# Performance work log

Measured on AMD Instinct MI355X. Metric: run time of the kernel, lower is better.

Reference implementation:

```python
import jax, jax.numpy as jnp
import numpy as np

TAU = 2.0      # LIF membrane time constant
ALPHA = 4.0    # spikingjelly surrogate.Sigmoid default alpha
EPS = 1e-5     # BatchNorm eps
HEADS = 8

@jax.custom_vjp
def heaviside(x):
    return (x >= 0).astype(x.dtype)

def _hv_fwd(x):
    return (x >= 0).astype(x.dtype), x

def _hv_bwd(x, g):
    s = jax.nn.sigmoid(ALPHA * x)
    return (g * ALPHA * s * (1.0 - s),)

heaviside.defvjp(_hv_fwd, _hv_bwd)

def lif(x, vth=1.0):
    # multi-step LIF, decay_input=True, v_reset=0 (hard reset), detach_reset=True
    def step(v, xt):
        v = v + (xt - v) / TAU
        s = heaviside(v - vth)
        v = v * (1.0 - jax.lax.stop_gradient(s))
        return v, s
    _, spikes = jax.lax.scan(step, jnp.zeros_like(x[0]), x)
    return spikes

def bn(x, gamma, beta, mean, var):
    # x: [T,B,C,N]; eval-mode BatchNorm1d over channel axis 2
    inv = gamma * jax.lax.rsqrt(var + EPS)
    return x * inv[None, None, :, None] + (beta - mean * inv)[None, None, :, None]

def conv1x1(x, w):
    # x: [T,B,C,N], w: [Cout,Cin] (Conv1d kernel_size=1)
    return jnp.einsum('tbcn,dc->tbdn', x, w)

def setup_inputs():
    key = jax.random.key(0)
    ks = jax.random.split(key, 24)
    T, B, C, H, W = 4, 16, 512, 32, 32
    scale = 1.0 / np.sqrt(C)
    d = {}
    d['x'] = jax.random.normal(ks[0], (T, B, C, H, W), jnp.float32)
    def bn_params(i):
        g = 1.0 + 0.1 * jax.random.normal(ks[i], (C,), jnp.float32)
        b = 0.1 * jax.random.normal(ks[i + 1], (C,), jnp.float32)
        m = 0.1 * jax.random.normal(ks[i + 2], (C,), jnp.float32)
        v = jax.random.uniform(ks[i + 3], (C,), jnp.float32, 0.5, 1.5)
        return g, b, m, v
    d['q_w'] = scale * jax.random.normal(ks[1], (C, C), jnp.float32)
    d['q_gamma'], d['q_beta'], d['q_mean'], d['q_var'] = bn_params(2)
    d['k_w'] = scale * jax.random.normal(ks[6], (C, C), jnp.float32)
    d['k_gamma'], d['k_beta'], d['k_mean'], d['k_var'] = bn_params(7)
    d['proj_w'] = scale * jax.random.normal(ks[11], (C, C), jnp.float32)
    d['proj_b'] = 0.01 * jax.random.normal(ks[12], (C,), jnp.float32)
    d['p_gamma'], d['p_beta'], d['p_mean'], d['p_var'] = bn_params(13)
    return d

def reference(x, q_w, q_gamma, q_beta, q_mean, q_var,
              k_w, k_gamma, k_beta, k_mean, k_var,
              proj_w, proj_b, p_gamma, p_beta, p_mean, p_var):
    T, B, C, H, W = x.shape
    N = H * W
    Dh = C // HEADS
    xs = lif(x).reshape(T, B, C, N)                    # shortcut_lif then flatten(3)
    q = lif(bn(conv1x1(xs, q_w), q_gamma, q_beta, q_mean, q_var))
    k = lif(bn(conv1x1(xs, k_w), k_gamma, k_beta, k_mean, k_var))
    qh = q.reshape(T, B, HEADS, Dh, N).sum(axis=3, keepdims=True)  # [T,B,h,1,N]
    attn = lif(qh, vth=0.5)
    kh = k.reshape(T, B, HEADS, Dh, N)
    y = (attn * kh).reshape(T, B, C, N)
    y = bn(conv1x1(y, proj_w) + proj_b[None, None, :, None],
           p_gamma, p_beta, p_mean, p_var)
    return y.reshape(T, B, C, H, W), attn
```

## Files before the change

### kernel.cpp

```cpp
#include <hip/hip_runtime.h>

typedef unsigned char u8;
typedef unsigned short u16;
typedef unsigned int u32;
typedef float f32x4 __attribute__((ext_vector_type(4)));
typedef short s16x8 __attribute__((ext_vector_type(8)));

#define T_ 4
#define B_ 16
#define C_ 512
#define N_ 1024
#define YSZ 33554432

__device__ __forceinline__ u16 f2bf(float f) {
  u32 u = __float_as_uint(f);
  u32 r = u + 0x7FFFu + ((u >> 16) & 1u);
  return (u16)(r >> 16);
}
__device__ __forceinline__ float bf2f(u16 h) { return __uint_as_float(((u32)h) << 16); }

__device__ __forceinline__ void async16(const void* g, void* l) {
  __builtin_amdgcn_global_load_lds((const __attribute__((address_space(1))) void*)g,
                                   (__attribute__((address_space(3))) void*)l, 16, 0, 0);
}

__device__ __forceinline__ s16x8 expand8(u32 m) {
  union { u32 w[4]; s16x8 v; } u;
  u.w[0] = (m & 1u   ? 0x3F80u : 0u) | (m & 2u   ? 0x3F800000u : 0u);
  u.w[1] = (m & 4u   ? 0x3F80u : 0u) | (m & 8u   ? 0x3F800000u : 0u);
  u.w[2] = (m & 16u  ? 0x3F80u : 0u) | (m & 32u  ? 0x3F800000u : 0u);
  u.w[3] = (m & 64u  ? 0x3F80u : 0u) | (m & 128u ? 0x3F800000u : 0u);
  return u.v;
}

__global__ void prep_kernel(const float* __restrict__ qw, const float* __restrict__ kw,
                            const float* __restrict__ pw,
                            const float* __restrict__ qg, const float* __restrict__ qb,
                            const float* __restrict__ qm, const float* __restrict__ qv,
                            const float* __restrict__ kg, const float* __restrict__ kb,
                            const float* __restrict__ km, const float* __restrict__ kv,
                            const float* __restrict__ pg, const float* __restrict__ pbt,
                            const float* __restrict__ pm, const float* __restrict__ pv,
                            u16* __restrict__ whlq, u16* __restrict__ whlk,
                            u16* __restrict__ pwb, float* __restrict__ consts) {
  int blk = blockIdx.x, tid = threadIdx.x;
  if (blk < 512) {
    int d = blk;
    for (int c = tid; c < 512; c += 256) {
      float w = qw[d * 512 + c];
      u16 hi = f2bf(w);
      whlq[d * 1024 + c] = hi;
      whlq[d * 1024 + 512 + c] = f2bf(w - bf2f(hi));
      w = kw[d * 512 + c];
      hi = f2bf(w);
      whlk[d * 1024 + c] = hi;
      whlk[d * 1024 + 512 + c] = f2bf(w - bf2f(hi));
      pwb[d * 512 + c] = f2bf(pw[d * 512 + c]);
    }
  } else {
    for (int c = tid; c < 512; c += 256) {
      float inv = qg[c] / sqrtf(qv[c] + 1e-5f);
      consts[c] = inv; consts[512 + c] = qb[c] - qm[c] * inv;
      inv = kg[c] / sqrtf(kv[c] + 1e-5f);
      consts[1024 + c] = inv; consts[1536 + c] = kb[c] - km[c] * inv;
      inv = pg[c] / sqrtf(pv[c] + 1e-5f);
      consts[2048 + c] = inv; consts[2560 + c] = pbt[c] - pm[c] * inv;
    }
  }
}

__global__ __launch_bounds__(256) void lifx_kernel(const float* __restrict__ x,
                                                   u8* __restrict__ xsb) {
  int b = blockIdx.z;
  int cbase = blockIdx.y * 64, nbase = blockIdx.x * 64;
  int tid = threadIdx.x;
  int c_l = tid >> 6, n_l = tid & 63;
  float v[16];
#pragma unroll
  for (int i = 0; i < 16; ++i) v[i] = 0.f;
  for (int t = 0; t < 4; ++t) {
    const float* xp = x + ((size_t)(t * 16 + b) * 512 + cbase + c_l * 16) * 1024 + nbase + n_l;
    u32 mask = 0;
#pragma unroll
    for (int i = 0; i < 16; ++i) {
      float xv = xp[(size_t)i * 1024];
      float vn = v[i] + 0.5f * (xv - v[i]);
      bool s = vn >= 1.0f;
      mask |= (s ? 1u : 0u) << i;
      v[i] = s ? 0.f : vn;
    }
    *(u16*)&xsb[((size_t)(t * 16 + b) * 1024 + nbase + n_l) * 64 + (cbase >> 3) + c_l * 2] =
        (u16)mask;
  }
}

__global__ __launch_bounds__(256, 4) void gemm_q_kernel(
    const u16* __restrict__ A, const u8* __restrict__ xsb,
    const float* __restrict__ consts, float* __restrict__ dout) {
  const int tid = threadIdx.x;
  const int lane = tid & 63, w = tid >> 6;
  const int quad = lane >> 4, l16 = lane & 15;
  const int b = blockIdx.z;
  const int m_blk = blockIdx.y * 64, n_blk = blockIdx.x * 128;
  const int srow = lane >> 3;
  const int scol = (((lane & 7) ^ srow) & 7) * 8;
  __shared__ __align__(16) u16 smem[2 * 4096];
  u16* Ash = smem;
  u16* Asl = smem + 4096;
  const int rxor = l16 & 7;
  const int row0 = n_blk + w * 32 + l16;
  const int row1 = row0 + 16;
  float v[32];
#pragma unroll
  for (int i = 0; i < 32; ++i) v[i] = 0.f;
  float va[2] = {0.f, 0.f};

  for (int t = 0; t < 4; ++t) {
    f32x4 acc[4][2];
    const f32x4 zero = {0.f, 0.f, 0.f, 0.f};
#pragma unroll
    for (int i = 0; i < 4; ++i)
#pragma unroll
      for (int j = 0; j < 2; ++j) acc[i][j] = zero;
    const u8* bitsT = xsb + (size_t)(t * 16 + b) * (N_ * 64);

    for (int k0 = 0; k0 < 512; k0 += 64) {
#pragma unroll
      for (int i = 0; i < 2; ++i) {
        int r = i * 32 + w * 8 + srow;
        int lo = (i * 32 + w * 8) * 64;
        async16(A + (size_t)(m_blk + r) * 1024 + k0 + scol, &Ash[lo]);
        async16(A + (size_t)(m_blk + r) * 1024 + 512 + k0 + scol, &Asl[lo]);
      }
      uint2 g0 = *(const uint2*)&bitsT[(size_t)row0 * 64 + (k0 >> 3)];
      uint2 g1 = *(const uint2*)&bitsT[(size_t)row1 * 64 + (k0 >> 3)];
      __syncthreads();
#pragma unroll
      for (int kk = 0; kk < 2; ++kk) {
        s16x8 ah[4], al[4], bf[2];
        const int slot = ((kk * 4 + quad) ^ rxor) * 8;
#pragma unroll
        for (int ti = 0; ti < 4; ++ti) {
          ah[ti] = *(const s16x8*)&Ash[(ti * 16 + l16) * 64 + slot];
          al[ti] = *(const s16x8*)&Asl[(ti * 16 + l16) * 64 + slot];
        }
        u32 w0 = kk ? g0.y : g0.x;
        u32 w1 = kk ? g1.y : g1.x;
        bf[0] = expand8((w0 >> (quad * 8)) & 0xFFu);
        bf[1] = expand8((w1 >> (quad * 8)) & 0xFFu);
#pragma unroll
        for (int ti = 0; ti < 4; ++ti)
#pragma unroll
          for (int tj = 0; tj < 2; ++tj) {
            acc[ti][tj] = __builtin_amdgcn_mfma_f32_16x16x32_bf16(ah[ti], bf[tj], acc[ti][tj], 0, 0, 0);
            acc[ti][tj] = __builtin_amdgcn_mfma_f32_16x16x32_bf16(al[ti], bf[tj], acc[ti][tj], 0, 0, 0);
          }
      }
      __syncthreads();
    }

    float qp[2] = {0.f, 0.f};
#pragma unroll
    for (int ti = 0; ti < 4; ++ti) {
#pragma unroll
      for (int r = 0; r < 4; ++r) {
        int row = m_blk + ti * 16 + quad * 4 + r;
        float iv = consts[row], ib = consts[512 + row];
#pragma unroll
        for (int tj = 0; tj < 2; ++tj) {
          float bnv = acc[ti][tj][r] * iv + ib;
          float vv = v[(ti * 2 + tj) * 4 + r];
          float vn = vv + 0.5f * (bnv - vv);
          bool s = vn >= 1.0f;
          v[(ti * 2 + tj) * 4 + r] = s ? 0.f : vn;
          qp[tj] += s ? 1.f : 0.f;
        }
      }
    }
    int h = m_blk >> 6;
#pragma unroll
    for (int tj = 0; tj < 2; ++tj) {
      float q = qp[tj];
      q += __shfl_xor(q, 16, 64);
      q += __shfl_xor(q, 32, 64);
      float vn = va[tj] + 0.5f * (q - va[tj]);
      bool s = vn >= 0.5f;
      va[tj] = s ? 0.f : vn;
      if (quad == 0) {
        int col = n_blk + w * 32 + tj * 16 + l16;
        dout[(size_t)YSZ + ((size_t)(t * 16 + b) * 8 + h) * 1024 + col] = s ? 1.f : 0.f;
      }
    }
  }
}

__global__ __launch_bounds__(256, 4) void gemm_k_kernel(
    const u16* __restrict__ A, const u8* __restrict__ xsb,
    const float* __restrict__ consts, const float* __restrict__ dout,
    u8* __restrict__ y2b) {
  const int tid = threadIdx.x;
  const int lane = tid & 63, w = tid >> 6;
  const int quad = lane >> 4, l16 = lane & 15;
  const int b = blockIdx.z;
  const int m_blk = blockIdx.y * 64, n_blk = blockIdx.x * 128;
  const int srow = lane >> 3;
  const int scol = (((lane & 7) ^ srow) & 7) * 8;
  __shared__ __align__(16) u16 smem[9216];
  u16* Ash = smem;
  u16* Asl = smem + 4096;
  u16* Ys  = smem;
  const int rxor = l16 & 7;
  const int row0 = n_blk + w * 32 + l16;
  const int row1 = row0 + 16;
  float v[32];
#pragma unroll
  for (int i = 0; i < 32; ++i) v[i] = 0.f;

  for (int t = 0; t < 4; ++t) {
    f32x4 acc[4][2];
    const f32x4 zero = {0.f, 0.f, 0.f, 0.f};
#pragma unroll
    for (int i = 0; i < 4; ++i)
#pragma unroll
      for (int j = 0; j < 2; ++j) acc[i][j] = zero;
    const u8* bitsT = xsb + (size_t)(t * 16 + b) * (N_ * 64);

    for (int k0 = 0; k0 < 512; k0 += 64) {
#pragma unroll
      for (int i = 0; i < 2; ++i) {
        int r = i * 32 + w * 8 + srow;
        int lo = (i * 32 + w * 8) * 64;
        async16(A + (size_t)(m_blk + r) * 1024 + k0 + scol, &Ash[lo]);
        async16(A + (size_t)(m_blk + r) * 1024 + 512 + k0 + scol, &Asl[lo]);
      }
      uint2 g0 = *(const uint2*)&bitsT[(size_t)row0 * 64 + (k0 >> 3)];
      uint2 g1 = *(const uint2*)&bitsT[(size_t)row1 * 64 + (k0 >> 3)];
      __syncthreads();
#pragma unroll
      for (int kk = 0; kk < 2; ++kk) {
        s16x8 ah[4], al[4], bf[2];
        const int slot = ((kk * 4 + quad) ^ rxor) * 8;
#pragma unroll
        for (int ti = 0; ti < 4; ++ti) {
          ah[ti] = *(const s16x8*)&Ash[(ti * 16 + l16) * 64 + slot];
          al[ti] = *(const s16x8*)&Asl[(ti * 16 + l16) * 64 + slot];
        }
        u32 w0 = kk ? g0.y : g0.x;
        u32 w1 = kk ? g1.y : g1.x;
        bf[0] = expand8((w0 >> (quad * 8)) & 0xFFu);
        bf[1] = expand8((w1 >> (quad * 8)) & 0xFFu);
#pragma unroll
        for (int ti = 0; ti < 4; ++ti)
#pragma unroll
          for (int tj = 0; tj < 2; ++tj) {
            acc[ti][tj] = __builtin_amdgcn_mfma_f32_16x16x32_bf16(ah[ti], bf[tj], acc[ti][tj], 0, 0, 0);
            acc[ti][tj] = __builtin_amdgcn_mfma_f32_16x16x32_bf16(al[ti], bf[tj], acc[ti][tj], 0, 0, 0);
          }
      }
      __syncthreads();
    }

    int h = m_blk >> 6;
    float at[2];
#pragma unroll
    for (int tj = 0; tj < 2; ++tj) {
      int col = n_blk + w * 32 + tj * 16 + l16;
      at[tj] = dout[(size_t)YSZ + ((size_t)(t * 16 + b) * 8 + h) * 1024 + col];
    }

#pragma unroll
    for (int ti = 0; ti < 4; ++ti) {
      u16 pk[2][4];
#pragma unroll
      for (int r = 0; r < 4; ++r) {
        int row = m_blk + ti * 16 + quad * 4 + r;
        float iv = consts[1024 + row], ib = consts[1536 + row];
#pragma unroll
        for (int tj = 0; tj < 2; ++tj) {
          float bnv = acc[ti][tj][r] * iv + ib;
          float vv = v[(ti * 2 + tj) * 4 + r];
          float vn = vv + 0.5f * (bnv - vv);
          bool s = vn >= 1.0f;
          v[(ti * 2 + tj) * 4 + r] = s ? 0.f : vn;
          pk[tj][r] = (s && at[tj] != 0.f) ? 0x3F80 : 0;
        }
      }
#pragma unroll
      for (int tj = 0; tj < 2; ++tj) {
        int n_loc = w * 32 + tj * 16 + l16;
        int c_loc = ti * 16 + quad * 4;
        u32 lo2 = (u32)pk[tj][0] | ((u32)pk[tj][1] << 16);
        u32 hi2 = (u32)pk[tj][2] | ((u32)pk[tj][3] << 16);
        uint2 pv2; pv2.x = lo2; pv2.y = hi2;
        *(uint2*)&Ys[n_loc * 72 + c_loc] = pv2;
      }
    }
    __syncthreads();
    u8* yb = y2b + ((size_t)(t * 16 + b) * 1024 + n_blk) * 64 + (m_blk >> 3);
#pragma unroll
    for (int p = 0; p < 4; ++p) {
      int idx = p * 256 + tid;
      int rown = idx >> 3, bc = idx & 7;
      uint4 q = *(const uint4*)&Ys[rown * 72 + bc * 8];
      u32 byte = ((q.x >> 7) & 1u) | (((q.x >> 23) & 1u) << 1) |
                 (((q.y >> 7) & 1u) << 2) | (((q.y >> 23) & 1u) << 3) |
                 (((q.z >> 7) & 1u) << 4) | (((q.z >> 23) & 1u) << 5) |
                 (((q.w >> 7) & 1u) << 6) | (((q.w >> 23) & 1u) << 7);
      yb[(size_t)rown * 64 + bc] = (u8)byte;
    }
    __syncthreads();
  }
}

__global__ __launch_bounds__(256, 3) void gemm_proj_kernel(
    const u16* __restrict__ A, const u8* __restrict__ y2b,
    float* __restrict__ outP, const float* __restrict__ projb,
    const float* __restrict__ consts) {
  const int tid = threadIdx.x;
  const int lane = tid & 63, w = tid >> 6;
  const int wm = w >> 1, wn = w & 1;
  const int quad = lane >> 4, l16 = lane & 15;
  const int tb = blockIdx.z;
  const int m_blk = blockIdx.y * 128, n_blk = blockIdx.x * 128;
  const int srow = lane >> 3;
  const int scol = (((lane & 7) ^ srow) & 7) * 8;
  __shared__ __align__(16) u16 As[128 * 64];
  f32x4 acc[4][4];
  const f32x4 zero = {0.f, 0.f, 0.f, 0.f};
#pragma unroll
  for (int i = 0; i < 4; ++i)
#pragma unroll
    for (int j = 0; j < 4; ++j) acc[i][j] = zero;
  const u8* bitsT = y2b + (size_t)tb * (N_ * 64);
  const int rxor = l16 & 7;
  const int browb = n_blk + wn * 64 + l16;

  for (int k0 = 0; k0 < 512; k0 += 64) {
#pragma unroll
    for (int i = 0; i < 4; ++i) {
      int r = i * 32 + w * 8 + srow;
      async16(A + (size_t)(m_blk + r) * 512 + k0 + scol, &As[(i * 32 + w * 8) * 64]);
    }
    uint2 g[4];
#pragma unroll
    for (int tj = 0; tj < 4; ++tj)
      g[tj] = *(const uint2*)&bitsT[(size_t)(browb + tj * 16) * 64 + (k0 >> 3)];
    __syncthreads();
#pragma unroll
    for (int kk = 0; kk < 2; ++kk) {
      s16x8 af[4], bf[4];
      const int slot = ((kk * 4 + quad) ^ rxor) * 8;
#pragma unroll
      for (int ti = 0; ti < 4; ++ti)
        af[ti] = *(const s16x8*)&As[(wm * 64 + ti * 16 + l16) * 64 + slot];
#pragma unroll
      for (int tj = 0; tj < 4; ++tj) {
        u32 wbits = kk ? g[tj].y : g[tj].x;
        bf[tj] = expand8((wbits >> (quad * 8)) & 0xFFu);
      }
#pragma unroll
      for (int ti = 0; ti < 4; ++ti)
#pragma unroll
        for (int tj = 0; tj < 4; ++tj)
          acc[ti][tj] = __builtin_amdgcn_mfma_f32_16x16x32_bf16(af[ti], bf[tj], acc[ti][tj], 0, 0, 0);
    }
    __syncthreads();
  }

  const float* pinv = consts + 2048;
  const float* pb2 = consts + 2560;
  float* o = outP + (size_t)tb * (C_ * N_);
#pragma unroll
  for (int ti = 0; ti < 4; ++ti) {
    int row0 = m_blk + wm * 64 + ti * 16 + quad * 4;
#pragma unroll
    for (int r = 0; r < 4; ++r) {
      int row = row0 + r;
      float bi = projb[row], piv = pinv[row], pbi = pb2[row];
#pragma unroll
      for (int tj = 0; tj < 4; ++tj) {
        int col = n_blk + wn * 64 + tj * 16 + l16;
        o[(size_t)row * N_ + col] = (acc[ti][tj][r] + bi) * piv + pbi;
      }
    }
  }
}

extern "C" void kernel_launch(void* const* d_in, const int* in_sizes, int n_in,
                              void* d_out, int out_size, void* d_ws, size_t ws_size,
                              hipStream_t stream) {
  const float* x   = (const float*)d_in[0];
  const float* qw  = (const float*)d_in[1];
  const float* qg  = (const float*)d_in[2];
  const float* qb  = (const float*)d_in[3];
  const float* qm  = (const float*)d_in[4];
  const float* qv  = (const float*)d_in[5];
  const float* kw  = (const float*)d_in[6];
  const float* kg  = (const float*)d_in[7];
  const float* kb  = (const float*)d_in[8];
  const float* km  = (const float*)d_in[9];
  const float* kv  = (const float*)d_in[10];
  const float* pw  = (const float*)d_in[11];
  const float* pb  = (const float*)d_in[12];
  const float* pg  = (const float*)d_in[13];
  const float* pbt = (const float*)d_in[14];
  const float* pm  = (const float*)d_in[15];
  const float* pv  = (const float*)d_in[16];
  float* out = (float*)d_out;
  char* ws = (char*)d_ws;

  u8*  xsb      = (u8*)ws;
  u8*  y2b      = (u8*)(ws + 4194304);
  u16* whlq     = (u16*)(ws + 8388608);
  u16* whlk     = (u16*)(ws + 9437184);
  u16* pwb      = (u16*)(ws + 10485760);
  float* consts = (float*)(ws + 11010048);

  prep_kernel<<<513, 256, 0, stream>>>(qw, kw, pw, qg, qb, qm, qv, kg, kb, km, kv,
                                       pg, pbt, pm, pv, whlq, whlk, pwb, consts);
  lifx_kernel<<<dim3(16, 8, 16), 256, 0, stream>>>(x, xsb);
  gemm_q_kernel<<<dim3(8, 8, 16), 256, 0, stream>>>(whlq, xsb, consts, out);
  gemm_k_kernel<<<dim3(8, 8, 16), 256, 0, stream>>>(whlk, xsb, consts, out, y2b);
  gemm_proj_kernel<<<dim3(8, 4, 64), 256, 0, stream>>>(pwb, y2b, out, pb, consts);
}
```

Measured before the change: 467.4 us.

## Share weight tiles across all timesteps with double-buffered 128x128 Q/K GEMM blocks

```diff
diff --git a/kernel.cpp b/kernel.cpp
--- a/kernel.cpp
+++ b/kernel.cpp
@@ -94,81 +94,124 @@
   }
 }
 
-__global__ __launch_bounds__(256, 4) void gemm_q_kernel(
+__device__ __forceinline__ void qk_mainloop_allt(
+    const u16* __restrict__ A, const u8* __restrict__ xsb, u16* sm,
+    int b, int m_blk, int n_blk, int wid, int wm, int wn,
+    int quad, int l16, int srow, int scol, int rxor,
+    f32x4 (&acc)[4][4][2]) {
+  const int arow = wid * 8 + srow;
+  const u8* bbase = xsb + ((size_t)b * N_ + n_blk + wn * 32 + l16) * 64;
+
+#pragma unroll
+  for (int i = 0; i < 2; ++i) {
+    int r = i * 64 + arow;
+    int lo = (i * 64 + wid * 8) * 64;
+    async16(A + (size_t)(m_blk + r) * 1024 + scol, &sm[lo]);
+    async16(A + (size_t)(m_blk + r) * 1024 + 512 + scol, &sm[8192 + lo]);
+  }
+  uint2 g[4][2], gN[4][2];
+#pragma unroll
+  for (int t = 0; t < 4; ++t)
+#pragma unroll
+    for (int tj = 0; tj < 2; ++tj)
+      g[t][tj] = *(const uint2*)(bbase + (size_t)t * 1048576 + tj * 1024);
+  __syncthreads();
+
+  int cur = 0;
+  for (int s = 0; s < 8; ++s) {
+    if (s < 7) {
+      const int k0n = (s + 1) * 64;
+      u16* D = sm + (cur ^ 1) * 16384;
+#pragma unroll
+      for (int i = 0; i < 2; ++i) {
+        int r = i * 64 + arow;
+        int lo = (i * 64 + wid * 8) * 64;
+        async16(A + (size_t)(m_blk + r) * 1024 + k0n + scol, &D[lo]);
+        async16(A + (size_t)(m_blk + r) * 1024 + 512 + k0n + scol, &D[8192 + lo]);
+      }
+#pragma unroll
+      for (int t = 0; t < 4; ++t)
+#pragma unroll
+        for (int tj = 0; tj < 2; ++tj)
+          gN[t][tj] = *(const uint2*)(bbase + (size_t)t * 1048576 + tj * 1024 + (k0n >> 3));
+    }
+    const u16* Ash = sm + cur * 16384;
+    const u16* Asl = Ash + 8192;
+#pragma unroll
+    for (int kk = 0; kk < 2; ++kk) {
+      s16x8 ah[4], al[4];
+      const int slot = ((kk * 4 + quad) ^ rxor) * 8;
+#pragma unroll
+      for (int ti = 0; ti < 4; ++ti) {
+        ah[ti] = *(const s16x8*)&Ash[(wm * 64 + ti * 16 + l16) * 64 + slot];
+        al[ti] = *(const s16x8*)&Asl[(wm * 64 + ti * 16 + l16) * 64 + slot];
+      }
+#pragma unroll
+      for (int t = 0; t < 4; ++t) {
+        s16x8 bf0 = expand8(((kk ? g[t][0].y : g[t][0].x) >> (quad * 8)) & 0xFFu);
+        s16x8 bf1 = expand8(((kk ? g[t][1].y : g[t][1].x) >> (quad * 8)) & 0xFFu);
+#pragma unroll
+        for (int ti = 0; ti < 4; ++ti) {
+          acc[t][ti][0] = __builtin_amdgcn_mfma_f32_16x16x32_bf16(ah[ti], bf0, acc[t][ti][0], 0, 0, 0);
+          acc[t][ti][0] = __builtin_amdgcn_mfma_f32_16x16x32_bf16(al[ti], bf0, acc[t][ti][0], 0, 0, 0);
+          acc[t][ti][1] = __builtin_amdgcn_mfma_f32_16x16x32_bf16(ah[ti], bf1, acc[t][ti][1], 0, 0, 0);
+          acc[t][ti][1] = __builtin_amdgcn_mfma_f32_16x16x32_bf16(al[ti], bf1, acc[t][ti][1], 0, 0, 0);
+        }
+      }
+    }
+    __syncthreads();
+    if (s < 7) {
+#pragma unroll
+      for (int t = 0; t < 4; ++t)
+#pragma unroll
+        for (int tj = 0; tj < 2; ++tj) g[t][tj] = gN[t][tj];
+    }
+    cur ^= 1;
+  }
+}
+
+__global__ __launch_bounds__(512, 2) void gemm_q_kernel(
     const u16* __restrict__ A, const u8* __restrict__ xsb,
     const float* __restrict__ consts, float* __restrict__ dout) {
+  extern __shared__ u16 sm[];
   const int tid = threadIdx.x;
-  const int lane = tid & 63, w = tid >> 6;
+  const int lane = tid & 63, wid = tid >> 6;
+  const int wm = wid >> 2, wn = wid & 3;
   const int quad = lane >> 4, l16 = lane & 15;
   const int b = blockIdx.z;
-  const int m_blk = blockIdx.y * 64, n_blk = blockIdx.x * 128;
+  const int m_blk = blockIdx.y * 128, n_blk = blockIdx.x * 128;
   const int srow = lane >> 3;
   const int scol = (((lane & 7) ^ srow) & 7) * 8;
-  __shared__ __align__(16) u16 smem[2 * 4096];
-  u16* Ash = smem;
-  u16* Asl = smem + 4096;
   const int rxor = l16 & 7;
-  const int row0 = n_blk + w * 32 + l16;
-  const int row1 = row0 + 16;
+
+  f32x4 acc[4][4][2];
+  const f32x4 zero = {0.f, 0.f, 0.f, 0.f};
+#pragma unroll
+  for (int t = 0; t < 4; ++t)
+#pragma unroll
+    for (int i = 0; i < 4; ++i)
+#pragma unroll
+      for (int j = 0; j < 2; ++j) acc[t][i][j] = zero;
+
+  qk_mainloop_allt(A, xsb, sm, b, m_blk, n_blk, wid, wm, wn, quad, l16, srow, scol, rxor, acc);
+
   float v[32];
 #pragma unroll
   for (int i = 0; i < 32; ++i) v[i] = 0.f;
   float va[2] = {0.f, 0.f};
-
+  const int h = (m_blk >> 6) + wm;
+#pragma unroll
   for (int t = 0; t < 4; ++t) {
-    f32x4 acc[4][2];
-    const f32x4 zero = {0.f, 0.f, 0.f, 0.f};
-#pragma unroll
-    for (int i = 0; i < 4; ++i)
-#pragma unroll
-      for (int j = 0; j < 2; ++j) acc[i][j] = zero;
-    const u8* bitsT = xsb + (size_t)(t * 16 + b) * (N_ * 64);
-
-    for (int k0 = 0; k0 < 512; k0 += 64) {
-#pragma unroll
-      for (int i = 0; i < 2; ++i) {
-        int r = i * 32 + w * 8 + srow;
-        int lo = (i * 32 + w * 8) * 64;
-        async16(A + (size_t)(m_blk + r) * 1024 + k0 + scol, &Ash[lo]);
-        async16(A + (size_t)(m_blk + r) * 1024 + 512 + k0 + scol, &Asl[lo]);
-      }
-      uint2 g0 = *(const uint2*)&bitsT[(size_t)row0 * 64 + (k0 >> 3)];
-      uint2 g1 = *(const uint2*)&bitsT[(size_t)row1 * 64 + (k0 >> 3)];
-      __syncthreads();
-#pragma unroll
-      for (int kk = 0; kk < 2; ++kk) {
-        s16x8 ah[4], al[4], bf[2];
-        const int slot = ((kk * 4 + quad) ^ rxor) * 8;
-#pragma unroll
-        for (int ti = 0; ti < 4; ++ti) {
-          ah[ti] = *(const s16x8*)&Ash[(ti * 16 + l16) * 64 + slot];
-          al[ti] = *(const s16x8*)&Asl[(ti * 16 + l16) * 64 + slot];
-        }
-        u32 w0 = kk ? g0.y : g0.x;
-        u32 w1 = kk ? g1.y : g1.x;
-        bf[0] = expand8((w0 >> (quad * 8)) & 0xFFu);
-        bf[1] = expand8((w1 >> (quad * 8)) & 0xFFu);
-#pragma unroll
-        for (int ti = 0; ti < 4; ++ti)
-#pragma unroll
-          for (int tj = 0; tj < 2; ++tj) {
-            acc[ti][tj] = __builtin_amdgcn_mfma_f32_16x16x32_bf16(ah[ti], bf[tj], acc[ti][tj], 0, 0, 0);
-            acc[ti][tj] = __builtin_amdgcn_mfma_f32_16x16x32_bf16(al[ti], bf[tj], acc[ti][tj], 0, 0, 0);
-          }
-      }
-      __syncthreads();
-    }
-
     float qp[2] = {0.f, 0.f};
 #pragma unroll
     for (int ti = 0; ti < 4; ++ti) {
 #pragma unroll
       for (int r = 0; r < 4; ++r) {
-        int row = m_blk + ti * 16 + quad * 4 + r;
+        int row = m_blk + wm * 64 + ti * 16 + quad * 4 + r;
         float iv = consts[row], ib = consts[512 + row];
 #pragma unroll
         for (int tj = 0; tj < 2; ++tj) {
-          float bnv = acc[ti][tj][r] * iv + ib;
+          float bnv = acc[t][ti][tj][r] * iv + ib;
           float vv = v[(ti * 2 + tj) * 4 + r];
           float vn = vv + 0.5f * (bnv - vv);
           bool s = vn >= 1.0f;
@@ -177,7 +220,6 @@
         }
       }
     }
-    int h = m_blk >> 6;
 #pragma unroll
     for (int tj = 0; tj < 2; ++tj) {
       float q = qp[tj];
@@ -187,126 +229,86 @@
       bool s = vn >= 0.5f;
       va[tj] = s ? 0.f : vn;
       if (quad == 0) {
-        int col = n_blk + w * 32 + tj * 16 + l16;
+        int col = n_blk + wn * 32 + tj * 16 + l16;
         dout[(size_t)YSZ + ((size_t)(t * 16 + b) * 8 + h) * 1024 + col] = s ? 1.f : 0.f;
       }
     }
   }
 }
 
-__global__ __launch_bounds__(256, 4) void gemm_k_kernel(
+__global__ __launch_bounds__(512, 2) void gemm_k_kernel(
     const u16* __restrict__ A, const u8* __restrict__ xsb,
     const float* __restrict__ consts, const float* __restrict__ dout,
     u8* __restrict__ y2b) {
+  extern __shared__ u16 sm[];
   const int tid = threadIdx.x;
-  const int lane = tid & 63, w = tid >> 6;
+  const int lane = tid & 63, wid = tid >> 6;
+  const int wm = wid >> 2, wn = wid & 3;
   const int quad = lane >> 4, l16 = lane & 15;
   const int b = blockIdx.z;
-  const int m_blk = blockIdx.y * 64, n_blk = blockIdx.x * 128;
+  const int m_blk = blockIdx.y * 128, n_blk = blockIdx.x * 128;
   const int srow = lane >> 3;
   const int scol = (((lane & 7) ^ srow) & 7) * 8;
-  __shared__ __align__(16) u16 smem[9216];
-  u16* Ash = smem;
-  u16* Asl = smem + 4096;
-  u16* Ys  = smem;
   const int rxor = l16 & 7;
-  const int row0 = n_blk + w * 32 + l16;
-  const int row1 = row0 + 16;
+
+  f32x4 acc[4][4][2];
+  const f32x4 zero = {0.f, 0.f, 0.f, 0.f};
+#pragma unroll
+  for (int t = 0; t < 4; ++t)
+#pragma unroll
+    for (int i = 0; i < 4; ++i)
+#pragma unroll
+      for (int j = 0; j < 2; ++j) acc[t][i][j] = zero;
+
+  qk_mainloop_allt(A, xsb, sm, b, m_blk, n_blk, wid, wm, wn, quad, l16, srow, scol, rxor, acc);
+
+  u16* Ysb = sm;
   float v[32];
 #pragma unroll
   for (int i = 0; i < 32; ++i) v[i] = 0.f;
-
+  const int h = (m_blk >> 6) + wm;
+#pragma unroll
   for (int t = 0; t < 4; ++t) {
-    f32x4 acc[4][2];
-    const f32x4 zero = {0.f, 0.f, 0.f, 0.f};
-#pragma unroll
-    for (int i = 0; i < 4; ++i)
-#pragma unroll
-      for (int j = 0; j < 2; ++j) acc[i][j] = zero;
-    const u8* bitsT = xsb + (size_t)(t * 16 + b) * (N_ * 64);
-
-    for (int k0 = 0; k0 < 512; k0 += 64) {
-#pragma unroll
-      for (int i = 0; i < 2; ++i) {
-        int r = i * 32 + w * 8 + srow;
-        int lo = (i * 32 + w * 8) * 64;
-        async16(A + (size_t)(m_blk + r) * 1024 + k0 + scol, &Ash[lo]);
-        async16(A + (size_t)(m_blk + r) * 1024 + 512 + k0 + scol, &Asl[lo]);
-      }
-      uint2 g0 = *(const uint2*)&bitsT[(size_t)row0 * 64 + (k0 >> 3)];
-      uint2 g1 = *(const uint2*)&bitsT[(size_t)row1 * 64 + (k0 >> 3)];
-      __syncthreads();
-#pragma unroll
-      for (int kk = 0; kk < 2; ++kk) {
-        s16x8 ah[4], al[4], bf[2];
-        const int slot = ((kk * 4 + quad) ^ rxor) * 8;
-#pragma unroll
-        for (int ti = 0; ti < 4; ++ti) {
-          ah[ti] = *(const s16x8*)&Ash[(ti * 16 + l16) * 64 + slot];
-          al[ti] = *(const s16x8*)&Asl[(ti * 16 + l16) * 64 + slot];
-        }
-        u32 w0 = kk ? g0.y : g0.x;
-        u32 w1 = kk ? g1.y : g1.x;
-        bf[0] = expand8((w0 >> (quad * 8)) & 0xFFu);
-        bf[1] = expand8((w1 >> (quad * 8)) & 0xFFu);
-#pragma unroll
-        for (int ti = 0; ti < 4; ++ti)
-#pragma unroll
-          for (int tj = 0; tj < 2; ++tj) {
-            acc[ti][tj] = __builtin_amdgcn_mfma_f32_16x16x32_bf16(ah[ti], bf[tj], acc[ti][tj], 0, 0, 0);
-            acc[ti][tj] = __builtin_amdgcn_mfma_f32_16x16x32_bf16(al[ti], bf[tj], acc[ti][tj], 0, 0, 0);
-          }
-      }
-      __syncthreads();
-    }
-
-    int h = m_blk >> 6;
     float at[2];
 #pragma unroll
     for (int tj = 0; tj < 2; ++tj) {
-      int col = n_blk + w * 32 + tj * 16 + l16;
+      int col = n_blk + wn * 32 + tj * 16 + l16;
       at[tj] = dout[(size_t)YSZ + ((size_t)(t * 16 + b) * 8 + h) * 1024 + col];
     }
-
 #pragma unroll
     for (int ti = 0; ti < 4; ++ti) {
-      u16 pk[2][4];
+      u32 nib[2] = {0u, 0u};
 #pragma unroll
       for (int r = 0; r < 4; ++r) {
-        int row = m_blk + ti * 16 + quad * 4 + r;
+        int row = m_blk + wm * 64 + ti * 16 + quad * 4 + r;
         float iv = consts[1024 + row], ib = consts[1536 + row];
 #pragma unroll
         for (int tj = 0; tj < 2; ++tj) {
-          float bnv = acc[ti][tj][r] * iv + ib;
+          float bnv = acc[t][ti][tj][r] * iv + ib;
           float vv = v[(ti * 2 + tj) * 4 + r];
           float vn = vv + 0.5f * (bnv - vv);
           bool s = vn >= 1.0f;
           v[(ti * 2 + tj) * 4 + r] = s ? 0.f : vn;
-          pk[tj][r] = (s && at[tj] != 0.f) ? 0x3F80 : 0;
+          nib[tj] |= (s && at[tj] != 0.f) ? (1u << r) : 0u;
         }
       }
 #pragma unroll
       for (int tj = 0; tj < 2; ++tj) {
-        int n_loc = w * 32 + tj * 16 + l16;
-        int c_loc = ti * 16 + quad * 4;
-        u32 lo2 = (u32)pk[tj][0] | ((u32)pk[tj][1] << 16);
-        u32 hi2 = (u32)pk[tj][2] | ((u32)pk[tj][3] << 16);
-        uint2 pv2; pv2.x = lo2; pv2.y = hi2;
-        *(uint2*)&Ys[n_loc * 72 + c_loc] = pv2;
+        u32 v16 = nib[tj] | (((u32)__shfl_xor((int)nib[tj], 16, 64)) << 4);
+        v16 = v16 | (((u32)__shfl_xor((int)v16, 32, 64)) << 8);
+        if (quad == 0) {
+          int n_loc = wn * 32 + tj * 16 + l16;
+          Ysb[n_loc * 10 + wm * 4 + ti] = (u16)v16;
+        }
       }
     }
     __syncthreads();
-    u8* yb = y2b + ((size_t)(t * 16 + b) * 1024 + n_blk) * 64 + (m_blk >> 3);
-#pragma unroll
-    for (int p = 0; p < 4; ++p) {
-      int idx = p * 256 + tid;
-      int rown = idx >> 3, bc = idx & 7;
-      uint4 q = *(const uint4*)&Ys[rown * 72 + bc * 8];
-      u32 byte = ((q.x >> 7) & 1u) | (((q.x >> 23) & 1u) << 1) |
-                 (((q.y >> 7) & 1u) << 2) | (((q.y >> 23) & 1u) << 3) |
-                 (((q.z >> 7) & 1u) << 4) | (((q.z >> 23) & 1u) << 5) |
-                 (((q.w >> 7) & 1u) << 6) | (((q.w >> 23) & 1u) << 7);
-      yb[(size_t)rown * 64 + bc] = (u8)byte;
+    {
+      u8* yb = y2b + ((size_t)(t * 16 + b) * 1024 + n_blk) * 64 + (m_blk >> 3);
+      int rown = tid >> 2, part = tid & 3;
+      const u16* src = &Ysb[rown * 10 + part * 2];
+      u32 pv = (u32)src[0] | ((u32)src[1] << 16);
+      *(u32*)&yb[(size_t)rown * 64 + part * 4] = pv;
     }
     __syncthreads();
   }
@@ -416,10 +418,19 @@
   u16* pwb      = (u16*)(ws + 10485760);
   float* consts = (float*)(ws + 11010048);
 
+  static int attr_done = 0;
+  if (!attr_done) {
+    hipFuncSetAttribute((const void*)gemm_q_kernel,
+                        hipFuncAttributeMaxDynamicSharedMemorySize, 65536);
+    hipFuncSetAttribute((const void*)gemm_k_kernel,
+                        hipFuncAttributeMaxDynamicSharedMemorySize, 65536);
+    attr_done = 1;
+  }
+
   prep_kernel<<<513, 256, 0, stream>>>(qw, kw, pw, qg, qb, qm, qv, kg, kb, km, kv,
                                        pg, pbt, pm, pv, whlq, whlk, pwb, consts);
   lifx_kernel<<<dim3(16, 8, 16), 256, 0, stream>>>(x, xsb);
-  gemm_q_kernel<<<dim3(8, 8, 16), 256, 0, stream>>>(whlq, xsb, consts, out);
-  gemm_k_kernel<<<dim3(8, 8, 16), 256, 0, stream>>>(whlk, xsb, consts, out, y2b);
+  gemm_q_kernel<<<dim3(8, 4, 16), 512, 65536, stream>>>(whlq, xsb, consts, out);
+  gemm_k_kernel<<<dim3(8, 4, 16), 512, 65536, stream>>>(whlk, xsb, consts, out, y2b);
   gemm_proj_kernel<<<dim3(8, 4, 64), 256, 0, stream>>>(pwb, y2b, out, pb, consts);
 }
```

New measurement: 401.2 us. -14.2%, faster.
